# Kernel tuning notes

Hardware: AMD Instinct MI355X
Metric: run time of the kernel (lower is better)

Reference implementation:

```python
import jax, jax.numpy as jnp
import numpy as np

TOP_K = 2  # module default top_k


def setup_inputs() -> dict:
    key = jax.random.key(0)
    k1, k2, k3 = jax.random.split(key, 3)
    B, D, E = 4096, 1024, 64  # tokens, input_dim, num_experts
    return {
        "tensor1": jax.random.normal(k1, (B, D), dtype=jnp.float32),
        "tensor2": jax.random.normal(k2, (B, D), dtype=jnp.float32),
        "gate_weight": jax.random.normal(k3, (E, 2 * D), dtype=jnp.float32) * 0.02,
    }


def reference(tensor1, tensor2, gate_weight):
    # x: (B, 2D)
    x = jnp.concatenate((tensor1, tensor2), axis=-1)
    # pairwise L2 distance between each token and each expert vector
    diff = gate_weight[None, :, :] - x[:, None, :]          # (B, E, 2D)
    logits = -jnp.sqrt(jnp.sum(diff * diff, axis=-1))        # (B, E)
    topk_logits, indices = jax.lax.top_k(logits, TOP_K)      # (B, K)
    gating_weights = jax.nn.softmax(topk_logits, axis=-1)    # (B, K)
    rows = jnp.arange(logits.shape[0])[:, None]              # (B, 1)
    sparse_gating = jnp.zeros_like(logits).at[rows, indices].set(gating_weights)
    return sparse_gating
```

## Files before the change

### kernel.cpp

```cpp
#include <hip/hip_runtime.h>
#include <math.h>

#define NTOK 4096
#define NDIM 1024
#define KTOT 2048
#define NEXP 64
#define TPB_TOK 32
#define KBLK 1024
#define NWAVE 8
#define KCH  (KBLK / NWAVE)
#define NSTEP (KCH / 32)
#define RS   68
#define NTILE (NTOK / TPB_TOK)

typedef _Float16 half8 __attribute__((ext_vector_type(8)));
typedef float    floatx4 __attribute__((ext_vector_type(4)));

#define XSCALE 16.0f
#define WSCALE 1024.0f
#define INVSCALE (1.0f / (16.0f * 1024.0f))

struct h2pair { _Float16 h, l; };
__device__ __forceinline__ h2pair split2(float v) {
    h2pair r;
    r.h = (_Float16)v;
    r.l = (_Float16)(v - (float)r.h);
    return r;
}

__global__ __launch_bounds__(256) void prep_w(const float* __restrict__ W,
                                              _Float16* __restrict__ WhT,
                                              _Float16* __restrict__ WlT,
                                              float* __restrict__ nrm) {
    const int e = blockIdx.x, t = threadIdx.x;
    const float* row = W + (size_t)e * KTOT + t * 8;
    const float4 a = *reinterpret_cast<const float4*>(row);
    const float4 b = *reinterpret_cast<const float4*>(row + 4);
    float ss = fmaf(a.x, a.x, fmaf(a.y, a.y, fmaf(a.z, a.z, fmaf(a.w, a.w, 0.f))));
    ss = fmaf(b.x, b.x, fmaf(b.y, b.y, fmaf(b.z, b.z, fmaf(b.w, b.w, ss))));

    const h2pair p0 = split2(a.x * WSCALE), p1 = split2(a.y * WSCALE);
    const h2pair p2 = split2(a.z * WSCALE), p3 = split2(a.w * WSCALE);
    const h2pair p4 = split2(b.x * WSCALE), p5 = split2(b.y * WSCALE);
    const h2pair p6 = split2(b.z * WSCALE), p7 = split2(b.w * WSCALE);
    half8 h, l;
    h[0]=p0.h; h[1]=p1.h; h[2]=p2.h; h[3]=p3.h; h[4]=p4.h; h[5]=p5.h; h[6]=p6.h; h[7]=p7.h;
    l[0]=p0.l; l[1]=p1.l; l[2]=p2.l; l[3]=p3.l; l[4]=p4.l; l[5]=p5.l; l[6]=p6.l; l[7]=p7.l;
    const size_t idx = ((size_t)t * NEXP + e) * 8;
    *reinterpret_cast<half8*>(WhT + idx) = h;
    *reinterpret_cast<half8*>(WlT + idx) = l;

    #pragma unroll
    for (int off = 32; off > 0; off >>= 1) ss += __shfl_down(ss, off, 64);
    __shared__ float red[4];
    const int lane = t & 63, wv = t >> 6;
    if (lane == 0) red[wv] = ss;
    __syncthreads();
    if (t == 0) nrm[e] = (red[0] + red[1]) + (red[2] + red[3]);
}

__global__ __launch_bounds__(512) void gate_main(const float* __restrict__ t1,
                                                 const float* __restrict__ t2,
                                                 const _Float16* __restrict__ WhT,
                                                 const _Float16* __restrict__ WlT,
                                                 float* __restrict__ dotp,
                                                 float* __restrict__ xnp) {
    __shared__ float Sd[NWAVE][TPB_TOK * RS];
    __shared__ float Cn[NWAVE][TPB_TOK];

    const int tid  = threadIdx.x;
    const int lane = tid & 63;
    const int wv   = tid >> 6;
    const int bid  = blockIdx.x;
    const int tile = bid >> 1;
    const int kb   = bid & 1;
    const int tok0 = tile * TPB_TOK;
    const int kbase = kb * KBLK + wv * KCH;
    const int n  = lane & 15;
    const int fq = lane >> 4;

    const float* __restrict__ xsrc = (kbase < NDIM) ? t1 : t2;
    const int koff = (kbase < NDIM) ? kbase : (kbase - NDIM);
    const float* __restrict__ xb0 = xsrc + (size_t)(tok0 + n) * NDIM + koff + fq * 8;
    const float* __restrict__ xb1 = xsrc + (size_t)(tok0 + 16 + n) * NDIM + koff + fq * 8;
    const _Float16* __restrict__ whb = WhT + ((size_t)(kbase >> 3) + fq) * (NEXP * 8) + n * 8;
    const _Float16* __restrict__ wlb = WlT + ((size_t)(kbase >> 3) + fq) * (NEXP * 8) + n * 8;

    floatx4 acc[2][4];
    #pragma unroll
    for (int tt = 0; tt < 2; ++tt)
        #pragma unroll
        for (int j = 0; j < 4; ++j) { acc[tt][j][0]=0.f; acc[tt][j][1]=0.f; acc[tt][j][2]=0.f; acc[tt][j][3]=0.f; }
    float ss0a = 0.f, ss0b = 0.f, ss1a = 0.f, ss1b = 0.f;

    #pragma unroll
    for (int s = 0; s < NSTEP; ++s) {
        const float4 x00 = *reinterpret_cast<const float4*>(xb0 + s * 32);
        const float4 x01 = *reinterpret_cast<const float4*>(xb0 + s * 32 + 4);
        const float4 x10 = *reinterpret_cast<const float4*>(xb1 + s * 32);
        const float4 x11 = *reinterpret_cast<const float4*>(xb1 + s * 32 + 4);
        half8 bh[4], bl[4];
        #pragma unroll
        for (int j = 0; j < 4; ++j) {
            bh[j] = *reinterpret_cast<const half8*>(whb + (size_t)s * 4 * (NEXP * 8) + j * 128);
            bl[j] = *reinterpret_cast<const half8*>(wlb + (size_t)s * 4 * (NEXP * 8) + j * 128);
        }
        ss0a = fmaf(x00.x, x00.x, fmaf(x00.y, x00.y, fmaf(x00.z, x00.z, fmaf(x00.w, x00.w, ss0a))));
        ss0b = fmaf(x01.x, x01.x, fmaf(x01.y, x01.y, fmaf(x01.z, x01.z, fmaf(x01.w, x01.w, ss0b))));
        ss1a = fmaf(x10.x, x10.x, fmaf(x10.y, x10.y, fmaf(x10.z, x10.z, fmaf(x10.w, x10.w, ss1a))));
        ss1b = fmaf(x11.x, x11.x, fmaf(x11.y, x11.y, fmaf(x11.z, x11.z, fmaf(x11.w, x11.w, ss1b))));
        const h2pair q0 = split2(x00.x * XSCALE), q1 = split2(x00.y * XSCALE);
        const h2pair q2 = split2(x00.z * XSCALE), q3 = split2(x00.w * XSCALE);
        const h2pair q4 = split2(x01.x * XSCALE), q5 = split2(x01.y * XSCALE);
        const h2pair q6 = split2(x01.z * XSCALE), q7 = split2(x01.w * XSCALE);
        const h2pair r0 = split2(x10.x * XSCALE), r1 = split2(x10.y * XSCALE);
        const h2pair r2 = split2(x10.z * XSCALE), r3 = split2(x10.w * XSCALE);
        const h2pair r4 = split2(x11.x * XSCALE), r5 = split2(x11.y * XSCALE);
        const h2pair r6 = split2(x11.z * XSCALE), r7 = split2(x11.w * XSCALE);
        half8 ah0, al0, ah1, al1;
        ah0[0]=q0.h; ah0[1]=q1.h; ah0[2]=q2.h; ah0[3]=q3.h; ah0[4]=q4.h; ah0[5]=q5.h; ah0[6]=q6.h; ah0[7]=q7.h;
        al0[0]=q0.l; al0[1]=q1.l; al0[2]=q2.l; al0[3]=q3.l; al0[4]=q4.l; al0[5]=q5.l; al0[6]=q6.l; al0[7]=q7.l;
        ah1[0]=r0.h; ah1[1]=r1.h; ah1[2]=r2.h; ah1[3]=r3.h; ah1[4]=r4.h; ah1[5]=r5.h; ah1[6]=r6.h; ah1[7]=r7.h;
        al1[0]=r0.l; al1[1]=r1.l; al1[2]=r2.l; al1[3]=r3.l; al1[4]=r4.l; al1[5]=r5.l; al1[6]=r6.l; al1[7]=r7.l;
        #pragma unroll
        for (int j = 0; j < 4; ++j) {
            acc[0][j] = __builtin_amdgcn_mfma_f32_16x16x32_f16(ah0, bh[j], acc[0][j], 0, 0, 0);
            acc[1][j] = __builtin_amdgcn_mfma_f32_16x16x32_f16(ah1, bh[j], acc[1][j], 0, 0, 0);
        }
        #pragma unroll
        for (int j = 0; j < 4; ++j) {
            acc[0][j] = __builtin_amdgcn_mfma_f32_16x16x32_f16(al0, bh[j], acc[0][j], 0, 0, 0);
            acc[1][j] = __builtin_amdgcn_mfma_f32_16x16x32_f16(al1, bh[j], acc[1][j], 0, 0, 0);
        }
        #pragma unroll
        for (int j = 0; j < 4; ++j) {
            acc[0][j] = __builtin_amdgcn_mfma_f32_16x16x32_f16(ah0, bl[j], acc[0][j], 0, 0, 0);
            acc[1][j] = __builtin_amdgcn_mfma_f32_16x16x32_f16(ah1, bl[j], acc[1][j], 0, 0, 0);
        }
    }

    #pragma unroll
    for (int tt = 0; tt < 2; ++tt)
        #pragma unroll
        for (int j = 0; j < 4; ++j)
            #pragma unroll
            for (int i = 0; i < 4; ++i)
                Sd[wv][(tt * 16 + fq * 4 + i) * RS + 16 * j + n] = acc[tt][j][i];

    float ss0 = ss0a + ss0b, ss1 = ss1a + ss1b;
    ss0 += __shfl_xor(ss0, 16, 64);
    ss0 += __shfl_xor(ss0, 32, 64);
    ss1 += __shfl_xor(ss1, 16, 64);
    ss1 += __shfl_xor(ss1, 32, 64);
    if (lane < 16) { Cn[wv][lane] = ss0; Cn[wv][16 + lane] = ss1; }
    __syncthreads();

    #pragma unroll
    for (int tt = 0; tt < 4; ++tt) {
        const int t = wv * 4 + tt;
        float gsum = 0.f, csum = 0.f;
        #pragma unroll
        for (int w = 0; w < NWAVE; ++w) {
            gsum += Sd[w][t * RS + lane];
            csum += Cn[w][t];
        }
        dotp[((size_t)(tile * 2 + kb) * TPB_TOK + t) * NEXP + lane] = gsum;
        if (lane == 0) xnp[(size_t)(tile * 2 + kb) * TPB_TOK + t] = csum;
    }
}

__global__ __launch_bounds__(512) void finalize(const float* __restrict__ dotp,
                                                const float* __restrict__ xnp,
                                                const float* __restrict__ nrm,
                                                float* __restrict__ out) {
    const int tid  = threadIdx.x;
    const int lane = tid & 63;
    const int wv   = tid >> 6;
    const int tok  = blockIdx.x * 8 + wv;
    const int tile = tok >> 5;
    const int t    = tok & 31;

    const float g = dotp[((size_t)(tile * 2 + 0) * TPB_TOK + t) * NEXP + lane]
                  + dotp[((size_t)(tile * 2 + 1) * TPB_TOK + t) * NEXP + lane];
    const float c = xnp[(size_t)(tile * 2 + 0) * TPB_TOK + t]
                  + xnp[(size_t)(tile * 2 + 1) * TPB_TOK + t];
    const float S = fmaf(-2.f * INVSCALE, g, c) + nrm[lane];
    const float logit = -sqrtf(S);

    float v1 = logit; int i1 = lane;
    #pragma unroll
    for (int off = 32; off > 0; off >>= 1) {
        float ov = __shfl_xor(v1, off, 64);
        int   oi = __shfl_xor(i1, off, 64);
        if (ov > v1 || (ov == v1 && oi < i1)) { v1 = ov; i1 = oi; }
    }
    float v2 = (lane == i1) ? -__builtin_inff() : logit;
    int   i2 = lane;
    #pragma unroll
    for (int off = 32; off > 0; off >>= 1) {
        float ov = __shfl_xor(v2, off, 64);
        int   oi = __shfl_xor(i2, off, 64);
        if (ov > v2 || (ov == v2 && oi < i2)) { v2 = ov; i2 = oi; }
    }
    const float e2  = expf(v2 - v1);
    const float inv = 1.f / (1.f + e2);
    const float o = (lane == i1) ? inv : ((lane == i2) ? e2 * inv : 0.f);
    out[(size_t)tok * NEXP + lane] = o;
}

extern "C" void kernel_launch(void* const* d_in, const int* in_sizes, int n_in,
                              void* d_out, int out_size, void* d_ws, size_t ws_size,
                              hipStream_t stream) {
    const float* t1 = (const float*)d_in[0];
    const float* t2 = (const float*)d_in[1];
    const float* W  = (const float*)d_in[2];
    float* out = (float*)d_out;

    char* ws = (char*)d_ws;
    float*    nrm  = (float*)ws;
    _Float16* WhT  = (_Float16*)(nrm + NEXP);
    _Float16* WlT  = WhT + (size_t)NEXP * KTOT;
    float*    dotp = (float*)(WlT + (size_t)NEXP * KTOT);
    float*    xnp  = dotp + (size_t)NTILE * 2 * TPB_TOK * NEXP;

    prep_w<<<NEXP, 256, 0, stream>>>(W, WhT, WlT, nrm);
    gate_main<<<NTILE * 2, 512, 0, stream>>>(t1, t2, WhT, WlT, dotp, xnp);
    finalize<<<NTOK / 8, 512, 0, stream>>>(dotp, xnp, nrm, out);
}
```

Measured before the change: 84.87 us.

## Widen token tile to 64 and split K into four blocks

Each block now covers 64 tokens (four 16-row MFMA tiles per wave) and one 512-wide K quarter, where before it covered 32 tokens and a 1024-wide K half. The grid keeps the same 256 blocks. Each W fragment loaded from global memory now feeds twice as many MFMAs, which lowers weight traffic per FLOP. The costs are more accumulator registers (64 floats per lane), a larger shared-memory staging area (Sd grows to about 139 KB), and twice as many partial sums for finalize to read and add.

```diff
diff --git a/kernel.cpp b/kernel.cpp
--- a/kernel.cpp
+++ b/kernel.cpp
@@ -5,8 +5,8 @@
 #define NDIM 1024
 #define KTOT 2048
 #define NEXP 64
-#define TPB_TOK 32
-#define KBLK 1024
+#define TPB_TOK 64
+#define KBLK 512
 #define NWAVE 8
 #define KCH  (KBLK / NWAVE)
 #define NSTEP (KCH / 32)
@@ -72,100 +72,96 @@
     const int lane = tid & 63;
     const int wv   = tid >> 6;
     const int bid  = blockIdx.x;
-    const int tile = bid >> 1;
-    const int kb   = bid & 1;
+    const int tile = bid >> 2;
+    const int kq   = bid & 3;
     const int tok0 = tile * TPB_TOK;
-    const int kbase = kb * KBLK + wv * KCH;
+    const int kbase = kq * KBLK + wv * KCH;
     const int n  = lane & 15;
     const int fq = lane >> 4;
 
     const float* __restrict__ xsrc = (kbase < NDIM) ? t1 : t2;
     const int koff = (kbase < NDIM) ? kbase : (kbase - NDIM);
-    const float* __restrict__ xb0 = xsrc + (size_t)(tok0 + n) * NDIM + koff + fq * 8;
-    const float* __restrict__ xb1 = xsrc + (size_t)(tok0 + 16 + n) * NDIM + koff + fq * 8;
+    const float* __restrict__ xb = xsrc + (size_t)(tok0 + n) * NDIM + koff + fq * 8;
     const _Float16* __restrict__ whb = WhT + ((size_t)(kbase >> 3) + fq) * (NEXP * 8) + n * 8;
     const _Float16* __restrict__ wlb = WlT + ((size_t)(kbase >> 3) + fq) * (NEXP * 8) + n * 8;
 
-    floatx4 acc[2][4];
-    #pragma unroll
-    for (int tt = 0; tt < 2; ++tt)
+    floatx4 acc[4][4];
+    #pragma unroll
+    for (int tt = 0; tt < 4; ++tt)
         #pragma unroll
         for (int j = 0; j < 4; ++j) { acc[tt][j][0]=0.f; acc[tt][j][1]=0.f; acc[tt][j][2]=0.f; acc[tt][j][3]=0.f; }
-    float ss0a = 0.f, ss0b = 0.f, ss1a = 0.f, ss1b = 0.f;
+    float ssx[4] = {0.f, 0.f, 0.f, 0.f};
 
     #pragma unroll
     for (int s = 0; s < NSTEP; ++s) {
-        const float4 x00 = *reinterpret_cast<const float4*>(xb0 + s * 32);
-        const float4 x01 = *reinterpret_cast<const float4*>(xb0 + s * 32 + 4);
-        const float4 x10 = *reinterpret_cast<const float4*>(xb1 + s * 32);
-        const float4 x11 = *reinterpret_cast<const float4*>(xb1 + s * 32 + 4);
         half8 bh[4], bl[4];
         #pragma unroll
         for (int j = 0; j < 4; ++j) {
             bh[j] = *reinterpret_cast<const half8*>(whb + (size_t)s * 4 * (NEXP * 8) + j * 128);
             bl[j] = *reinterpret_cast<const half8*>(wlb + (size_t)s * 4 * (NEXP * 8) + j * 128);
         }
-        ss0a = fmaf(x00.x, x00.x, fmaf(x00.y, x00.y, fmaf(x00.z, x00.z, fmaf(x00.w, x00.w, ss0a))));
-        ss0b = fmaf(x01.x, x01.x, fmaf(x01.y, x01.y, fmaf(x01.z, x01.z, fmaf(x01.w, x01.w, ss0b))));
-        ss1a = fmaf(x10.x, x10.x, fmaf(x10.y, x10.y, fmaf(x10.z, x10.z, fmaf(x10.w, x10.w, ss1a))));
-        ss1b = fmaf(x11.x, x11.x, fmaf(x11.y, x11.y, fmaf(x11.z, x11.z, fmaf(x11.w, x11.w, ss1b))));
-        const h2pair q0 = split2(x00.x * XSCALE), q1 = split2(x00.y * XSCALE);
-        const h2pair q2 = split2(x00.z * XSCALE), q3 = split2(x00.w * XSCALE);
-        const h2pair q4 = split2(x01.x * XSCALE), q5 = split2(x01.y * XSCALE);
-        const h2pair q6 = split2(x01.z * XSCALE), q7 = split2(x01.w * XSCALE);
-        const h2pair r0 = split2(x10.x * XSCALE), r1 = split2(x10.y * XSCALE);
-        const h2pair r2 = split2(x10.z * XSCALE), r3 = split2(x10.w * XSCALE);
-        const h2pair r4 = split2(x11.x * XSCALE), r5 = split2(x11.y * XSCALE);
-        const h2pair r6 = split2(x11.z * XSCALE), r7 = split2(x11.w * XSCALE);
-        half8 ah0, al0, ah1, al1;
-        ah0[0]=q0.h; ah0[1]=q1.h; ah0[2]=q2.h; ah0[3]=q3.h; ah0[4]=q4.h; ah0[5]=q5.h; ah0[6]=q6.h; ah0[7]=q7.h;
-        al0[0]=q0.l; al0[1]=q1.l; al0[2]=q2.l; al0[3]=q3.l; al0[4]=q4.l; al0[5]=q5.l; al0[6]=q6.l; al0[7]=q7.l;
-        ah1[0]=r0.h; ah1[1]=r1.h; ah1[2]=r2.h; ah1[3]=r3.h; ah1[4]=r4.h; ah1[5]=r5.h; ah1[6]=r6.h; ah1[7]=r7.h;
-        al1[0]=r0.l; al1[1]=r1.l; al1[2]=r2.l; al1[3]=r3.l; al1[4]=r4.l; al1[5]=r5.l; al1[6]=r6.l; al1[7]=r7.l;
-        #pragma unroll
-        for (int j = 0; j < 4; ++j) {
-            acc[0][j] = __builtin_amdgcn_mfma_f32_16x16x32_f16(ah0, bh[j], acc[0][j], 0, 0, 0);
-            acc[1][j] = __builtin_amdgcn_mfma_f32_16x16x32_f16(ah1, bh[j], acc[1][j], 0, 0, 0);
+        half8 ah[4], al[4];
+        #pragma unroll
+        for (int tt = 0; tt < 4; ++tt) {
+            const float* xp = xb + (size_t)tt * 16 * NDIM + s * 32;
+            const float4 xa = *reinterpret_cast<const float4*>(xp);
+            const float4 xc = *reinterpret_cast<const float4*>(xp + 4);
+            ssx[tt] = fmaf(xa.x, xa.x, fmaf(xa.y, xa.y, fmaf(xa.z, xa.z, fmaf(xa.w, xa.w, ssx[tt]))));
+            ssx[tt] = fmaf(xc.x, xc.x, fmaf(xc.y, xc.y, fmaf(xc.z, xc.z, fmaf(xc.w, xc.w, ssx[tt]))));
+            const h2pair q0 = split2(xa.x * XSCALE), q1 = split2(xa.y * XSCALE);
+            const h2pair q2 = split2(xa.z * XSCALE), q3 = split2(xa.w * XSCALE);
+            const h2pair q4 = split2(xc.x * XSCALE), q5 = split2(xc.y * XSCALE);
+            const h2pair q6 = split2(xc.z * XSCALE), q7 = split2(xc.w * XSCALE);
+            ah[tt][0]=q0.h; ah[tt][1]=q1.h; ah[tt][2]=q2.h; ah[tt][3]=q3.h;
+            ah[tt][4]=q4.h; ah[tt][5]=q5.h; ah[tt][6]=q6.h; ah[tt][7]=q7.h;
+            al[tt][0]=q0.l; al[tt][1]=q1.l; al[tt][2]=q2.l; al[tt][3]=q3.l;
+            al[tt][4]=q4.l; al[tt][5]=q5.l; al[tt][6]=q6.l; al[tt][7]=q7.l;
         }
         #pragma unroll
-        for (int j = 0; j < 4; ++j) {
-            acc[0][j] = __builtin_amdgcn_mfma_f32_16x16x32_f16(al0, bh[j], acc[0][j], 0, 0, 0);
-            acc[1][j] = __builtin_amdgcn_mfma_f32_16x16x32_f16(al1, bh[j], acc[1][j], 0, 0, 0);
-        }
-        #pragma unroll
-        for (int j = 0; j < 4; ++j) {
-            acc[0][j] = __builtin_amdgcn_mfma_f32_16x16x32_f16(ah0, bl[j], acc[0][j], 0, 0, 0);
-            acc[1][j] = __builtin_amdgcn_mfma_f32_16x16x32_f16(ah1, bl[j], acc[1][j], 0, 0, 0);
-        }
-    }
-
-    #pragma unroll
-    for (int tt = 0; tt < 2; ++tt)
+        for (int j = 0; j < 4; ++j)
+            #pragma unroll
+            for (int tt = 0; tt < 4; ++tt)
+                acc[tt][j] = __builtin_amdgcn_mfma_f32_16x16x32_f16(ah[tt], bh[j], acc[tt][j], 0, 0, 0);
+        #pragma unroll
+        for (int j = 0; j < 4; ++j)
+            #pragma unroll
+            for (int tt = 0; tt < 4; ++tt)
+                acc[tt][j] = __builtin_amdgcn_mfma_f32_16x16x32_f16(al[tt], bh[j], acc[tt][j], 0, 0, 0);
+        #pragma unroll
+        for (int j = 0; j < 4; ++j)
+            #pragma unroll
+            for (int tt = 0; tt < 4; ++tt)
+                acc[tt][j] = __builtin_amdgcn_mfma_f32_16x16x32_f16(ah[tt], bl[j], acc[tt][j], 0, 0, 0);
+    }
+
+    #pragma unroll
+    for (int tt = 0; tt < 4; ++tt)
         #pragma unroll
         for (int j = 0; j < 4; ++j)
             #pragma unroll
             for (int i = 0; i < 4; ++i)
                 Sd[wv][(tt * 16 + fq * 4 + i) * RS + 16 * j + n] = acc[tt][j][i];
 
-    float ss0 = ss0a + ss0b, ss1 = ss1a + ss1b;
-    ss0 += __shfl_xor(ss0, 16, 64);
-    ss0 += __shfl_xor(ss0, 32, 64);
-    ss1 += __shfl_xor(ss1, 16, 64);
-    ss1 += __shfl_xor(ss1, 32, 64);
-    if (lane < 16) { Cn[wv][lane] = ss0; Cn[wv][16 + lane] = ss1; }
+    #pragma unroll
+    for (int tt = 0; tt < 4; ++tt) {
+        float ss = ssx[tt];
+        ss += __shfl_xor(ss, 16, 64);
+        ss += __shfl_xor(ss, 32, 64);
+        if (lane < 16) Cn[wv][tt * 16 + lane] = ss;
+    }
     __syncthreads();
 
     #pragma unroll
-    for (int tt = 0; tt < 4; ++tt) {
-        const int t = wv * 4 + tt;
+    for (int tt = 0; tt < 8; ++tt) {
+        const int t = wv * 8 + tt;
         float gsum = 0.f, csum = 0.f;
         #pragma unroll
         for (int w = 0; w < NWAVE; ++w) {
             gsum += Sd[w][t * RS + lane];
             csum += Cn[w][t];
         }
-        dotp[((size_t)(tile * 2 + kb) * TPB_TOK + t) * NEXP + lane] = gsum;
-        if (lane == 0) xnp[(size_t)(tile * 2 + kb) * TPB_TOK + t] = csum;
+        dotp[((size_t)(tile * 4 + kq) * TPB_TOK + t) * NEXP + lane] = gsum;
+        if (lane == 0) xnp[(size_t)(tile * 4 + kq) * TPB_TOK + t] = csum;
     }
 }
 
@@ -177,13 +173,15 @@
     const int lane = tid & 63;
     const int wv   = tid >> 6;
     const int tok  = blockIdx.x * 8 + wv;
-    const int tile = tok >> 5;
-    const int t    = tok & 31;
-
-    const float g = dotp[((size_t)(tile * 2 + 0) * TPB_TOK + t) * NEXP + lane]
-                  + dotp[((size_t)(tile * 2 + 1) * TPB_TOK + t) * NEXP + lane];
-    const float c = xnp[(size_t)(tile * 2 + 0) * TPB_TOK + t]
-                  + xnp[(size_t)(tile * 2 + 1) * TPB_TOK + t];
+    const int tile = tok >> 6;
+    const int t    = tok & 63;
+
+    float g = 0.f, c = 0.f;
+    #pragma unroll
+    for (int kq = 0; kq < 4; ++kq) {
+        g += dotp[((size_t)(tile * 4 + kq) * TPB_TOK + t) * NEXP + lane];
+        c += xnp[(size_t)(tile * 4 + kq) * TPB_TOK + t];
+    }
     const float S = fmaf(-2.f * INVSCALE, g, c) + nrm[lane];
     const float logit = -sqrtf(S);
 
@@ -221,9 +219,9 @@
     _Float16* WhT  = (_Float16*)(nrm + NEXP);
     _Float16* WlT  = WhT + (size_t)NEXP * KTOT;
     float*    dotp = (float*)(WlT + (size_t)NEXP * KTOT);
-    float*    xnp  = dotp + (size_t)NTILE * 2 * TPB_TOK * NEXP;
+    float*    xnp  = dotp + (size_t)NTILE * 4 * TPB_TOK * NEXP;
 
     prep_w<<<NEXP, 256, 0, stream>>>(W, WhT, WlT, nrm);
-    gate_main<<<NTILE * 2, 512, 0, stream>>>(t1, t2, WhT, WlT, dotp, xnp);
+    gate_main<<<NTILE * 4, 512, 0, stream>>>(t1, t2, WhT, WlT, dotp, xnp);
     finalize<<<NTOK / 8, 512, 0, stream>>>(dotp, xnp, nrm, out);
 }
```

Measured after the change: 87.48 us. 1.03x slower.
